# Optimization experiments

Measured on AMD Instinct MI355X. Metric: run time of the kernel, lower is better.

## Reference

```python
import jax, jax.numpy as jnp
import numpy as np

S, B, H, E, V, L = 64, 32, 1024, 512, 32000, 2


def setup_inputs() -> dict:
    key = jax.random.key(0)
    ks = jax.random.split(key, 12)
    dl = 1.0 / float(np.sqrt(H))
    u = lambda k, shape, a: jax.random.uniform(k, shape, minval=-a, maxval=a, dtype=jnp.float32)
    return {
        "inputs": jax.random.randint(ks[0], (S, B), 0, V),            # token ids [seq, batch]
        "hidden": jnp.zeros((L, B, H), jnp.float32),                  # init_hidden()
        "emb_W": u(ks[1], (V, E), 0.1),                               # embedding, uniform(-0.1,0.1)
        "Wx0": u(ks[2], (H, E), dl), "Wh0": u(ks[3], (H, H), dl), "bh0": u(ks[4], (H,), dl),
        "Wx1": u(ks[5], (H, H), dl), "Wh1": u(ks[6], (H, H), dl), "bh1": u(ks[7], (H,), dl),
        "Wout": u(ks[8], (V, H), 0.1),                                # output Linear, uniform(-0.1,0.1)
        "bout": jnp.zeros((V,), jnp.float32),                         # output bias zeros
    }


def reference(inputs, hidden, emb_W, Wx0, Wh0, bh0, Wx1, Wh1, bh1, Wout, bout):
    # Embedding lookup for all timesteps (dropout is identity at dp_keep_prob=1.0)
    x = emb_W[inputs]  # [S, B, E]
    Wxs = (Wx0, Wx1)
    Whs = (Wh0, Wh1)
    bs = (bh0, bh1)

    def step(h, x_t):
        # h: [L, B, H]; x_t: [B, E]
        out = x_t
        new_h = []
        for j in range(L):  # fixed small number of structurally distinct layers
            hj = jnp.tanh(out @ Wxs[j].T + h[j] @ Whs[j].T + bs[j])  # vanilla tanh RNN cell
            new_h.append(hj)
            out = hj
        return jnp.stack(new_h), out

    hidden_final, tops = jax.lax.scan(step, hidden, x)  # tops: [S, B, H]
    logits = tops @ Wout.T + bout                        # [S, B, V]
    return logits, hidden_final
```

## Files before the change

kernel.cpp:

```cpp
#include <hip/hip_runtime.h>
#include <hip/hip_bf16.h>

#define S_ 64
#define B_ 32
#define H_ 1024
#define E_ 512
#define V_ 32000

typedef unsigned short ushort_t;
typedef __attribute__((ext_vector_type(8))) short short8;
typedef __attribute__((ext_vector_type(4))) float f32x4;

__device__ __forceinline__ ushort_t f32_bf16(float x) {
    union { float f; unsigned u; } v; v.f = x;
    unsigned r = v.u + 0x7FFF + ((v.u >> 16) & 1);
    return (ushort_t)(r >> 16);
}

__device__ __forceinline__ float bf16_f32(ushort_t x) {
    union { unsigned u; float f; } v; v.u = ((unsigned)x) << 16;
    return v.f;
}

__global__ void cvt_bf16(const float* __restrict__ src, ushort_t* __restrict__ dst, int n4) {
    int i = blockIdx.x * blockDim.x + threadIdx.x;
    int stride = gridDim.x * blockDim.x;
    const float4* s4 = (const float4*)src;
    ushort4* d4 = (ushort4*)dst;
    for (; i < n4; i += stride) {
        float4 v = s4[i];
        ushort4 o;
        o.x = f32_bf16(v.x); o.y = f32_bf16(v.y);
        o.z = f32_bf16(v.z); o.w = f32_bf16(v.w);
        d4[i] = o;
    }
}

__global__ void init_hidden(const float* __restrict__ hid,
                            ushort_t* __restrict__ h0buf, ushort_t* __restrict__ h1buf) {
    int i = blockIdx.x * blockDim.x + threadIdx.x;
    int j = i & (B_ * H_ - 1);
    if (i < B_ * H_) h0buf[B_ * H_ + j] = f32_bf16(hid[i]);
    else             h1buf[B_ * H_ + j] = f32_bf16(hid[i]);
}

__global__ void gather_emb(const int* __restrict__ tok, const float* __restrict__ emb,
                           ushort_t* __restrict__ xb) {
    int m = blockIdx.x;
    int t = tok[m];
    const float4* src = (const float4*)(emb + (long)t * E_);
    ushort4* dst = (ushort4*)(xb + (long)m * E_);
    int i = threadIdx.x;
    float4 v = src[i];
    ushort4 o;
    o.x = f32_bf16(v.x); o.y = f32_bf16(v.y);
    o.z = f32_bf16(v.z); o.w = f32_bf16(v.w);
    dst[i] = o;
}

__global__ __launch_bounds__(256) void xproj_kernel(const ushort_t* __restrict__ Xb,
                                                    const ushort_t* __restrict__ Wx0b,
                                                    const float* __restrict__ bh0,
                                                    float* __restrict__ xproj) {
    int wid = (blockIdx.x * 256 + threadIdx.x) >> 6;
    int lane = threadIdx.x & 63;
    int quad = lane >> 4;
    int nt = wid & 63, mt = wid >> 6;
    int mrow = mt * 16 + (lane & 15);
    int nrow = nt * 16 + (lane & 15);
    const short8* Ap = (const short8*)(Xb + (long)mrow * E_ + quad * 8);
    const short8* Bp = (const short8*)(Wx0b + (long)nrow * E_ + quad * 8);
    f32x4 acc = {0.f, 0.f, 0.f, 0.f};
#pragma unroll
    for (int k = 0; k < E_ / 32; ++k)
        acc = __builtin_amdgcn_mfma_f32_16x16x32_bf16(Ap[k * 4], Bp[k * 4], acc, 0, 0, 0);
    float bias = bh0[nrow];
#pragma unroll
    for (int r = 0; r < 4; ++r) {
        int m = mt * 16 + quad * 4 + r;
        xproj[(long)m * H_ + nrow] = acc[r] + bias;
    }
}

__global__ __launch_bounds__(256) void step_kernel(const ushort_t* __restrict__ Wh0b,
                                                   const ushort_t* __restrict__ Wx1b,
                                                   const ushort_t* __restrict__ Wh1b,
                                                   const float* __restrict__ bh1,
                                                   const float* __restrict__ xproj,
                                                   ushort_t* __restrict__ h0buf,
                                                   ushort_t* __restrict__ h1buf,
                                                   ushort_t* __restrict__ tops,
                                                   int p) {
    int lb = blockIdx.x;
    int lane = threadIdx.x & 63;
    int widx = threadIdx.x >> 6;
    int quad = lane >> 4;
    if (lb < 32) {
        if (p >= S_) return;
        int wid = lb * 4 + widx;
        int nt = wid & 63, mt = wid >> 6;
        int b0 = mt * 16 + (lane & 15);
        int h = nt * 16 + (lane & 15);
        const ushort_t* Aprev = h0buf + ((p + 1) & 1) * (B_ * H_);
        const short8* Ap = (const short8*)(Aprev + (long)b0 * H_ + quad * 8);
        const short8* Wp = (const short8*)(Wh0b + (long)h * H_ + quad * 8);
        f32x4 acc = {0.f, 0.f, 0.f, 0.f};
#pragma unroll
        for (int k = 0; k < H_ / 32; ++k)
            acc = __builtin_amdgcn_mfma_f32_16x16x32_bf16(Ap[k * 4], Wp[k * 4], acc, 0, 0, 0);
        ushort_t* out = h0buf + (p & 1) * (B_ * H_);
        const float* xp = xproj + (long)p * B_ * H_;
#pragma unroll
        for (int r = 0; r < 4; ++r) {
            int b = mt * 16 + quad * 4 + r;
            float v = tanhf(acc[r] + xp[b * H_ + h]);
            out[b * H_ + h] = f32_bf16(v);
        }
    } else {
        if (p < 1) return;
        int t = p - 1;
        int wid = (lb - 32) * 4 + widx;
        int nt = wid & 63, mt = wid >> 6;
        int b0 = mt * 16 + (lane & 15);
        int h = nt * 16 + (lane & 15);
        const ushort_t* A0 = h0buf + (t & 1) * (B_ * H_);
        const ushort_t* A1 = h1buf + ((t + 1) & 1) * (B_ * H_);
        const short8* Ap0 = (const short8*)(A0 + (long)b0 * H_ + quad * 8);
        const short8* Wp0 = (const short8*)(Wx1b + (long)h * H_ + quad * 8);
        const short8* Ap1 = (const short8*)(A1 + (long)b0 * H_ + quad * 8);
        const short8* Wp1 = (const short8*)(Wh1b + (long)h * H_ + quad * 8);
        f32x4 acc = {0.f, 0.f, 0.f, 0.f};
#pragma unroll
        for (int k = 0; k < H_ / 32; ++k)
            acc = __builtin_amdgcn_mfma_f32_16x16x32_bf16(Ap0[k * 4], Wp0[k * 4], acc, 0, 0, 0);
#pragma unroll
        for (int k = 0; k < H_ / 32; ++k)
            acc = __builtin_amdgcn_mfma_f32_16x16x32_bf16(Ap1[k * 4], Wp1[k * 4], acc, 0, 0, 0);
        float bias = bh1[h];
        ushort_t* out = h1buf + (t & 1) * (B_ * H_);
        ushort_t* top = tops + (long)t * B_ * H_;
#pragma unroll
        for (int r = 0; r < 4; ++r) {
            int b = mt * 16 + quad * 4 + r;
            float v = tanhf(acc[r] + bias);
            ushort_t bv = f32_bf16(v);
            out[b * H_ + h] = bv;
            top[b * H_ + h] = bv;
        }
    }
}

#define BM 128
#define BN 128
#define BK 32

__device__ __forceinline__ void ld_lds16(const ushort_t* g, ushort_t* l) {
    __builtin_amdgcn_global_load_lds((const __attribute__((address_space(1))) void*)g,
                                     (__attribute__((address_space(3))) void*)l, 16, 0, 0);
}

__global__ __launch_bounds__(256) void out_gemm(const ushort_t* __restrict__ A,
                                                const ushort_t* __restrict__ Bw,
                                                const float* __restrict__ bout,
                                                float* __restrict__ C) {
    __shared__ __align__(16) ushort_t lA[BM * BK];
    __shared__ __align__(16) ushort_t lB[BN * BK];
    int mblk = blockIdx.x;
    int nblk = blockIdx.y;
    int tid = threadIdx.x;
    int lane = tid & 63;
    int w = tid >> 6;
    int quad = lane >> 4;
    int srow = tid >> 2;
    int skol = (tid & 3) * 8;
    const ushort_t* Ag = A + (long)(mblk * BM + srow) * H_ + skol;
    const ushort_t* Bg = Bw + (long)(nblk * BN + srow) * H_ + skol;
    ushort_t* lA0 = lA + tid * 8;
    ushort_t* lA1 = lA + 2048 + tid * 8;
    ushort_t* lB0 = lB + tid * 8;
    ushort_t* lB1 = lB + 2048 + tid * 8;

    int msub = (w & 1) * 64;
    int nsub = (w >> 1) * 64;
    f32x4 acc[4][4];
#pragma unroll
    for (int i = 0; i < 4; ++i)
#pragma unroll
        for (int j = 0; j < 4; ++j) acc[i][j] = (f32x4){0.f, 0.f, 0.f, 0.f};

    for (int k0 = 0; k0 < H_; k0 += BK) {
        ld_lds16(Ag + k0, lA0);
        ld_lds16(Ag + 64 * H_ + k0, lA1);
        ld_lds16(Bg + k0, lB0);
        ld_lds16(Bg + 64 * H_ + k0, lB1);
        __syncthreads();
        short8 af[4], bf[4];
#pragma unroll
        for (int i = 0; i < 4; ++i)
            af[i] = *(const short8*)&lA[(msub + i * 16 + (lane & 15)) * BK + quad * 8];
#pragma unroll
        for (int j = 0; j < 4; ++j)
            bf[j] = *(const short8*)&lB[(nsub + j * 16 + (lane & 15)) * BK + quad * 8];
#pragma unroll
        for (int i = 0; i < 4; ++i)
#pragma unroll
            for (int j = 0; j < 4; ++j)
                acc[i][j] = __builtin_amdgcn_mfma_f32_16x16x32_bf16(af[i], bf[j], acc[i][j], 0, 0, 0);
        __syncthreads();
    }

#pragma unroll
    for (int j = 0; j < 4; ++j) {
        int n = nblk * BN + nsub + j * 16 + (lane & 15);
        float bo = bout[n];
#pragma unroll
        for (int i = 0; i < 4; ++i) {
#pragma unroll
            for (int r = 0; r < 4; ++r) {
                int m = mblk * BM + msub + i * 16 + quad * 4 + r;
                C[(long)m * V_ + n] = acc[i][j][r] + bo;
            }
        }
    }
}

__global__ void final_hidden(const ushort_t* __restrict__ h0buf,
                             const ushort_t* __restrict__ h1buf,
                             float* __restrict__ out) {
    int i = blockIdx.x * blockDim.x + threadIdx.x;
    int j = i & (B_ * H_ - 1);
    ushort_t v = (i < B_ * H_) ? h0buf[B_ * H_ + j] : h1buf[B_ * H_ + j];
    out[(long)S_ * B_ * V_ + i] = bf16_f32(v);
}

extern "C" void kernel_launch(void* const* d_in, const int* in_sizes, int n_in,
                              void* d_out, int out_size, void* d_ws, size_t ws_size,
                              hipStream_t stream) {
    const int*   tok  = (const int*)d_in[0];
    const float* hid  = (const float*)d_in[1];
    const float* emb  = (const float*)d_in[2];
    const float* Wx0  = (const float*)d_in[3];
    const float* Wh0  = (const float*)d_in[4];
    const float* bh0  = (const float*)d_in[5];
    const float* Wx1  = (const float*)d_in[6];
    const float* Wh1  = (const float*)d_in[7];
    const float* bh1  = (const float*)d_in[8];
    const float* Wout = (const float*)d_in[9];
    const float* bout = (const float*)d_in[10];
    float* out = (float*)d_out;

    char* ws = (char*)d_ws;
    size_t off = 0;
    ushort_t* woutb = (ushort_t*)(ws + off); off += (size_t)V_ * H_ * 2;
    ushort_t* wh0b  = (ushort_t*)(ws + off); off += (size_t)H_ * H_ * 2;
    ushort_t* wx1b  = (ushort_t*)(ws + off); off += (size_t)H_ * H_ * 2;
    ushort_t* wh1b  = (ushort_t*)(ws + off); off += (size_t)H_ * H_ * 2;
    ushort_t* wx0b  = (ushort_t*)(ws + off); off += (size_t)H_ * E_ * 2;
    ushort_t* xb    = (ushort_t*)(ws + off); off += (size_t)S_ * B_ * E_ * 2;
    float*    xproj = (float*)(ws + off);    off += (size_t)S_ * B_ * H_ * 4;
    ushort_t* topsb = (ushort_t*)(ws + off); off += (size_t)S_ * B_ * H_ * 2;
    ushort_t* h0b   = (ushort_t*)(ws + off); off += (size_t)2 * B_ * H_ * 2;
    ushort_t* h1b   = (ushort_t*)(ws + off); off += (size_t)2 * B_ * H_ * 2;

    cvt_bf16<<<2048, 256, 0, stream>>>(Wout, woutb, V_ * H_ / 4);
    cvt_bf16<<<256, 256, 0, stream>>>(Wh0, wh0b, H_ * H_ / 4);
    cvt_bf16<<<256, 256, 0, stream>>>(Wx1, wx1b, H_ * H_ / 4);
    cvt_bf16<<<256, 256, 0, stream>>>(Wh1, wh1b, H_ * H_ / 4);
    cvt_bf16<<<128, 256, 0, stream>>>(Wx0, wx0b, H_ * E_ / 4);
    init_hidden<<<256, 256, 0, stream>>>(hid, h0b, h1b);
    gather_emb<<<S_ * B_, 128, 0, stream>>>(tok, emb, xb);
    xproj_kernel<<<2048, 256, 0, stream>>>(xb, wx0b, bh0, xproj);
    for (int p = 0; p <= S_; ++p)
        step_kernel<<<64, 256, 0, stream>>>(wh0b, wx1b, wh1b, bh1, xproj, h0b, h1b, topsb, p);
    out_gemm<<<dim3(16, 250), 256, 0, stream>>>(topsb, woutb, bout, out);
    final_hidden<<<256, 256, 0, stream>>>(h0b, h1b, out);
}
```

Measured before the change: 1.672 ms.

## Replace per-timestep step kernel launches with persistent kernel and grid barrier

```diff
diff --git a/kernel.cpp b/kernel.cpp
--- a/kernel.cpp
+++ b/kernel.cpp
@@ -82,71 +82,85 @@
     }
 }
 
-__global__ __launch_bounds__(256) void step_kernel(const ushort_t* __restrict__ Wh0b,
-                                                   const ushort_t* __restrict__ Wx1b,
-                                                   const ushort_t* __restrict__ Wh1b,
-                                                   const float* __restrict__ bh1,
-                                                   const float* __restrict__ xproj,
-                                                   ushort_t* __restrict__ h0buf,
-                                                   ushort_t* __restrict__ h1buf,
-                                                   ushort_t* __restrict__ tops,
-                                                   int p) {
-    int lb = blockIdx.x;
-    int lane = threadIdx.x & 63;
-    int widx = threadIdx.x >> 6;
-    int quad = lane >> 4;
-    if (lb < 32) {
-        if (p >= S_) return;
-        int wid = lb * 4 + widx;
-        int nt = wid & 63, mt = wid >> 6;
-        int b0 = mt * 16 + (lane & 15);
-        int h = nt * 16 + (lane & 15);
-        const ushort_t* Aprev = h0buf + ((p + 1) & 1) * (B_ * H_);
-        const short8* Ap = (const short8*)(Aprev + (long)b0 * H_ + quad * 8);
-        const short8* Wp = (const short8*)(Wh0b + (long)h * H_ + quad * 8);
-        f32x4 acc = {0.f, 0.f, 0.f, 0.f};
-#pragma unroll
-        for (int k = 0; k < H_ / 32; ++k)
-            acc = __builtin_amdgcn_mfma_f32_16x16x32_bf16(Ap[k * 4], Wp[k * 4], acc, 0, 0, 0);
-        ushort_t* out = h0buf + (p & 1) * (B_ * H_);
-        const float* xp = xproj + (long)p * B_ * H_;
-#pragma unroll
-        for (int r = 0; r < 4; ++r) {
-            int b = mt * 16 + quad * 4 + r;
-            float v = tanhf(acc[r] + xp[b * H_ + h]);
-            out[b * H_ + h] = f32_bf16(v);
+__global__ __launch_bounds__(256) void rnn_persistent(const ushort_t* __restrict__ Wh0b,
+                                                      const ushort_t* __restrict__ Wx1b,
+                                                      const ushort_t* __restrict__ Wh1b,
+                                                      const float* __restrict__ bh1,
+                                                      const float* __restrict__ xproj,
+                                                      ushort_t* __restrict__ h0buf,
+                                                      ushort_t* __restrict__ h1buf,
+                                                      ushort_t* __restrict__ tops,
+                                                      unsigned* __restrict__ bar) {
+    const int lb = blockIdx.x;
+    const int tid = threadIdx.x;
+    const int lane = tid & 63;
+    const int widx = tid >> 6;
+    const int quad = lane >> 4;
+    const bool is_l0 = (lb < 32);
+
+    int wid = (is_l0 ? lb : (lb - 32)) * 4 + widx;
+    const int nt = wid & 63, mt = wid >> 6;
+    const int b0 = mt * 16 + (lane & 15);
+    const int h  = nt * 16 + (lane & 15);
+    const short8* Wp_h0 = (const short8*)(Wh0b + (long)h * H_ + quad * 8);
+    const short8* Wp_x1 = (const short8*)(Wx1b + (long)h * H_ + quad * 8);
+    const short8* Wp_h1 = (const short8*)(Wh1b + (long)h * H_ + quad * 8);
+    const float bias1 = is_l0 ? 0.f : bh1[h];
+
+    for (int p = 0; p <= S_; ++p) {
+        if (is_l0) {
+            if (p < S_) {
+                const ushort_t* Aprev = h0buf + ((p + 1) & 1) * (B_ * H_);
+                const short8* Ap = (const short8*)(Aprev + (long)b0 * H_ + quad * 8);
+                f32x4 acc = {0.f, 0.f, 0.f, 0.f};
+#pragma unroll
+                for (int k = 0; k < H_ / 32; ++k)
+                    acc = __builtin_amdgcn_mfma_f32_16x16x32_bf16(Ap[k * 4], Wp_h0[k * 4], acc, 0, 0, 0);
+                ushort_t* out = h0buf + (p & 1) * (B_ * H_);
+                const float* xp = xproj + (long)p * B_ * H_;
+#pragma unroll
+                for (int r = 0; r < 4; ++r) {
+                    int b = mt * 16 + quad * 4 + r;
+                    float v = tanhf(acc[r] + xp[b * H_ + h]);
+                    out[b * H_ + h] = f32_bf16(v);
+                }
+            }
+        } else {
+            if (p >= 1) {
+                const int t = p - 1;
+                const ushort_t* A0 = h0buf + (t & 1) * (B_ * H_);
+                const ushort_t* A1 = h1buf + ((t + 1) & 1) * (B_ * H_);
+                const short8* Ap0 = (const short8*)(A0 + (long)b0 * H_ + quad * 8);
+                const short8* Ap1 = (const short8*)(A1 + (long)b0 * H_ + quad * 8);
+                f32x4 acc = {0.f, 0.f, 0.f, 0.f};
+#pragma unroll
+                for (int k = 0; k < H_ / 32; ++k)
+                    acc = __builtin_amdgcn_mfma_f32_16x16x32_bf16(Ap0[k * 4], Wp_x1[k * 4], acc, 0, 0, 0);
+#pragma unroll
+                for (int k = 0; k < H_ / 32; ++k)
+                    acc = __builtin_amdgcn_mfma_f32_16x16x32_bf16(Ap1[k * 4], Wp_h1[k * 4], acc, 0, 0, 0);
+                ushort_t* out = h1buf + (t & 1) * (B_ * H_);
+                ushort_t* top = tops + (long)t * B_ * H_;
+#pragma unroll
+                for (int r = 0; r < 4; ++r) {
+                    int b = mt * 16 + quad * 4 + r;
+                    float v = tanhf(acc[r] + bias1);
+                    ushort_t bv = f32_bf16(v);
+                    out[b * H_ + h] = bv;
+                    top[b * H_ + h] = bv;
+                }
+            }
         }
-    } else {
-        if (p < 1) return;
-        int t = p - 1;
-        int wid = (lb - 32) * 4 + widx;
-        int nt = wid & 63, mt = wid >> 6;
-        int b0 = mt * 16 + (lane & 15);
-        int h = nt * 16 + (lane & 15);
-        const ushort_t* A0 = h0buf + (t & 1) * (B_ * H_);
-        const ushort_t* A1 = h1buf + ((t + 1) & 1) * (B_ * H_);
-        const short8* Ap0 = (const short8*)(A0 + (long)b0 * H_ + quad * 8);
-        const short8* Wp0 = (const short8*)(Wx1b + (long)h * H_ + quad * 8);
-        const short8* Ap1 = (const short8*)(A1 + (long)b0 * H_ + quad * 8);
-        const short8* Wp1 = (const short8*)(Wh1b + (long)h * H_ + quad * 8);
-        f32x4 acc = {0.f, 0.f, 0.f, 0.f};
-#pragma unroll
-        for (int k = 0; k < H_ / 32; ++k)
-            acc = __builtin_amdgcn_mfma_f32_16x16x32_bf16(Ap0[k * 4], Wp0[k * 4], acc, 0, 0, 0);
-#pragma unroll
-        for (int k = 0; k < H_ / 32; ++k)
-            acc = __builtin_amdgcn_mfma_f32_16x16x32_bf16(Ap1[k * 4], Wp1[k * 4], acc, 0, 0, 0);
-        float bias = bh1[h];
-        ushort_t* out = h1buf + (t & 1) * (B_ * H_);
-        ushort_t* top = tops + (long)t * B_ * H_;
-#pragma unroll
-        for (int r = 0; r < 4; ++r) {
-            int b = mt * 16 + quad * 4 + r;
-            float v = tanhf(acc[r] + bias);
-            ushort_t bv = f32_bf16(v);
-            out[b * H_ + h] = bv;
-            top[b * H_ + h] = bv;
+        __threadfence();
+        __syncthreads();
+        if (tid == 0) {
+            __hip_atomic_fetch_add(bar, 1u, __ATOMIC_RELEASE, __HIP_MEMORY_SCOPE_AGENT);
+            const unsigned target = 64u * (unsigned)(p + 1);
+            while (__hip_atomic_load(bar, __ATOMIC_ACQUIRE, __HIP_MEMORY_SCOPE_AGENT) < target)
+                __builtin_amdgcn_s_sleep(1);
         }
+        __syncthreads();
+        __threadfence();
     }
 }
 
@@ -261,6 +275,10 @@
     ushort_t* topsb = (ushort_t*)(ws + off); off += (size_t)S_ * B_ * H_ * 2;
     ushort_t* h0b   = (ushort_t*)(ws + off); off += (size_t)2 * B_ * H_ * 2;
     ushort_t* h1b   = (ushort_t*)(ws + off); off += (size_t)2 * B_ * H_ * 2;
+    off = (off + 127) & ~(size_t)127;
+    unsigned* bar   = (unsigned*)(ws + off); off += 128;
+
+    hipMemsetAsync(bar, 0, 128, stream);
 
     cvt_bf16<<<2048, 256, 0, stream>>>(Wout, woutb, V_ * H_ / 4);
     cvt_bf16<<<256, 256, 0, stream>>>(Wh0, wh0b, H_ * H_ / 4);
@@ -270,8 +288,7 @@
     init_hidden<<<256, 256, 0, stream>>>(hid, h0b, h1b);
     gather_emb<<<S_ * B_, 128, 0, stream>>>(tok, emb, xb);
     xproj_kernel<<<2048, 256, 0, stream>>>(xb, wx0b, bh0, xproj);
-    for (int p = 0; p <= S_; ++p)
-        step_kernel<<<64, 256, 0, stream>>>(wh0b, wx1b, wh1b, bh1, xproj, h0b, h1b, topsb, p);
+    rnn_persistent<<<64, 256, 0, stream>>>(wh0b, wx1b, wh1b, bh1, xproj, h0b, h1b, topsb, bar);
     out_gemm<<<dim3(16, 250), 256, 0, stream>>>(topsb, woutb, bout, out);
     final_hidden<<<256, 256, 0, stream>>>(h0b, h1b, out);
 }
```

Result: slower. 2.378 ms (+42.3%).
